# Performance work log

Hardware: AMD Instinct MI355X
Metric: run time of the kernel (lower is better)

## Reference

```python
import jax, jax.numpy as jnp
import numpy as np

N, E, D, H, L = 10000, 80000, 1024, 8, 2
C = D // H          # 128 per-head channels
NEG = 0.2           # GATv2 default negative_slope


def setup_inputs() -> dict:
    k = jax.random.split(jax.random.key(0), 16)
    s = 0.02
    return {
        "x": jax.random.normal(k[0], (N, D), jnp.float32),
        "edge_index": jax.random.randint(k[1], (2, E), 0, N),
        "edge_attr": jax.random.randint(k[2], (E,), 0, 3),
        "node_types": jax.random.randint(k[3], (N,), 0, 5),
        "node_type_emb": s * jax.random.normal(k[4], (5, D), jnp.float32),
        "edge_type_emb": s * jax.random.normal(k[5], (3, D), jnp.float32),
        "Wl": s * jax.random.normal(k[6], (L, D, D), jnp.float32),
        "bl": jnp.zeros((L, D), jnp.float32),
        "Wr": s * jax.random.normal(k[7], (L, D, D), jnp.float32),
        "br": jnp.zeros((L, D), jnp.float32),
        "We": s * jax.random.normal(k[8], (L, D, D), jnp.float32),
        "att": s * jax.random.normal(k[9], (L, H, C), jnp.float32),
        "conv_bias": jnp.zeros((L, D), jnp.float32),
        "out_W": s * jax.random.normal(k[10], (D, D), jnp.float32),
        "out_b": jnp.zeros((D,), jnp.float32),
    }


def _gatv2(h, src, dst, ee, Wl, bl, Wr, br, We, att, b):
    """PyG GATv2Conv: concat=True, add_self_loops=True (fill_value='mean')."""
    n = h.shape[0]
    xl = (h @ Wl + bl).reshape(n, H, C)   # source transform (lin_l)
    xr = (h @ Wr + br).reshape(n, H, C)   # target transform (lin_r)
    # self loops: edge_attr of a loop = mean of raw incoming edge feats
    cnt = jax.ops.segment_sum(jnp.ones(src.shape, jnp.float32), dst, num_segments=n)
    loop_attr = jax.ops.segment_sum(ee, dst, num_segments=n) / jnp.maximum(cnt, 1.0)[:, None]
    loops = jnp.arange(n)
    s2 = jnp.concatenate([src, loops])
    d2 = jnp.concatenate([dst, loops])
    ea = jnp.concatenate([ee, loop_attr], axis=0)          # [E+N, D]
    ep = (ea @ We).reshape(-1, H, C)                        # lin_edge (no bias)
    e = jax.nn.leaky_relu(xl[s2] + xr[d2] + ep, NEG)        # [E+N, H, C]
    logit = jnp.einsum('ehc,hc->eh', e, att)                # attention logits
    # segment softmax over destination nodes (every node has a self loop)
    m = jax.ops.segment_max(logit, d2, num_segments=n)
    a = jnp.exp(logit - m[d2])
    alpha = a / jax.ops.segment_sum(a, d2, num_segments=n)[d2]
    out = jax.ops.segment_sum(alpha[:, :, None] * xl[s2], d2, num_segments=n)
    return out.reshape(n, D) + b


def reference(x, edge_index, edge_attr, node_types, node_type_emb, edge_type_emb,
              Wl, bl, Wr, br, We, att, conv_bias, out_W, out_b):
    h = x + node_type_emb[node_types]
    ee = edge_type_emb[edge_attr]
    src, dst = edge_index[0], edge_index[1]
    for i in range(L):  # num_layers = 2
        h = h + jax.nn.relu(_gatv2(h, src, dst, ee, Wl[i], bl[i], Wr[i], br[i],
                                   We[i], att[i], conv_bias[i]))
    return h @ out_W + out_b
```

## Files before the change

kernel.cpp:

```cpp
#include <hip/hip_runtime.h>
#include <hip/hip_bf16.h>
#include <stdint.h>

typedef __bf16 bf16_t;
typedef bf16_t bf16x8 __attribute__((ext_vector_type(8)));
typedef bf16_t bf16x4 __attribute__((ext_vector_type(4)));
typedef float f32x4 __attribute__((ext_vector_type(4)));

#define NN 10000
#define EE 80000
#define DD 1024
#define LL 2
#define MPAD 10112
#define NEGS 0.2f

#define GLOAD_LDS16(g, l) \
    __builtin_amdgcn_global_load_lds((__attribute__((address_space(1))) void*)(void*)(g), \
                                     (__attribute__((address_space(3))) void*)(l), 16, 0, 0)

__global__ __launch_bounds__(256)
void preamble(const float* __restrict__ Wl, const float* __restrict__ Wr,
              const float* __restrict__ outW, bf16_t* __restrict__ WT,
              bf16_t* __restrict__ OWT,
              const float* __restrict__ x, const int* __restrict__ ntypes,
              const float* __restrict__ nte, bf16_t* __restrict__ hbuf,
              const float* __restrict__ bl, const float* __restrict__ br,
              const float* __restrict__ outb, float* __restrict__ biasb,
              float* __restrict__ M3L, int* __restrict__ deg)
{
    __shared__ float tile[32][33];
    int b = blockIdx.x;
    int tid = threadIdx.x;
    if (b < 5120) {
        int z = b >> 10, rem = b & 1023;
        int bx = rem & 31, by = rem >> 5;
        const float* src;
        bf16_t* dstp;
        switch (z) {
            case 0: src = Wl;                       dstp = WT;                        break;
            case 1: src = Wr;                       dstp = WT + (size_t)1024*1024;    break;
            case 2: src = Wl + (size_t)1024*1024;   dstp = WT + (size_t)2*1024*1024;  break;
            case 3: src = Wr + (size_t)1024*1024;   dstp = WT + (size_t)3*1024*1024;  break;
            default: src = outW;                    dstp = OWT;                       break;
        }
        int tx = tid & 31, ty = tid >> 5;
#pragma unroll
        for (int i = 0; i < 4; ++i)
            tile[ty + i*8][tx] = src[(size_t)(by*32 + ty + i*8)*1024 + bx*32 + tx];
        __syncthreads();
#pragma unroll
        for (int i = 0; i < 4; ++i)
            dstp[(size_t)(bx*32 + ty + i*8)*1024 + by*32 + tx] = (bf16_t)tile[tx][ty + i*8];
    } else if (b < 10176) {
        size_t idx = ((size_t)(b - 5120)*256 + tid) * 8;
        if (idx >= (size_t)MPAD*1024) return;
        int n = (int)(idx >> 10);
        int c = (int)(idx & 1023);
        bf16x8 outv;
        if (n < NN) {
            const float* xp = x + (size_t)n*1024 + c;
            int t = ntypes[n];
            const float* ep = nte + (size_t)t*1024 + c;
#pragma unroll
            for (int j = 0; j < 8; ++j) outv[j] = (bf16_t)(xp[j] + ep[j]);
        } else {
#pragma unroll
            for (int j = 0; j < 8; ++j) outv[j] = (bf16_t)0.f;
        }
        *(bf16x8*)(hbuf + idx) = outv;
    } else if (b < 10196) {
        int i = (b - 10176)*256 + tid;
        if (i < 4096) {
            int l = i >> 11, j = i & 2047;
            biasb[i] = (j < 1024) ? bl[l*1024 + j] : br[l*1024 + j - 1024];
        } else if (i < 5120) {
            biasb[i] = outb[i - 4096];
        }
    } else if (b < 10220) {
        int i = (b - 10196)*256 + tid;
        if (i < LL*3072) M3L[i] = 0.f;
    } else {
        int i = (b - 10220)*256 + tid;
        if (i < NN) deg[i] = 0;
    }
}

__global__ __launch_bounds__(256)
void compute_m3_all(const float* __restrict__ ete, const float* __restrict__ We,
                    float* __restrict__ M3L)
{
    int l   = blockIdx.x >> 8;
    int bid = blockIdx.x & 255;
    const float* WeL = We + (size_t)l*1024*1024;
    float* M3 = M3L + l*3072;
    int j  = (bid & 3) * 256 + threadIdx.x;
    int k0 = (bid >> 2) * 16;
    float a0 = 0.f, a1 = 0.f, a2 = 0.f;
#pragma unroll
    for (int kk = 0; kk < 16; ++kk) {
        int k = k0 + kk;
        float w = WeL[(size_t)k*1024 + j];
        a0 += ete[k]        * w;
        a1 += ete[1024 + k] * w;
        a2 += ete[2048 + k] * w;
    }
    atomicAdd(&M3[j],        a0);
    atomicAdd(&M3[1024 + j], a1);
    atomicAdd(&M3[2048 + j], a2);
}

__global__ void hist_k(const int* __restrict__ dsts, int* __restrict__ deg)
{ int e = blockIdx.x*256 + threadIdx.x; if (e < EE) atomicAdd(&deg[dsts[e]], 1); }

__global__ __launch_bounds__(1024)
void scan_csr(const int* __restrict__ deg, int* __restrict__ rp, int* __restrict__ cursor)
{
    __shared__ int tot[1024];
    int t = threadIdx.x;
    int base = t * 10;
    int v[10];
    int run = 0;
#pragma unroll
    for (int j = 0; j < 10; ++j) {
        int i = base + j;
        int d = (i < NN) ? deg[i] : 0;
        run += d;
        v[j] = run;
    }
    tot[t] = run;
    __syncthreads();
    for (int d = 1; d < 1024; d <<= 1) {
        int xv = (t >= d) ? tot[t - d] : 0;
        __syncthreads();
        tot[t] += xv;
        __syncthreads();
    }
    int ex = (t == 0) ? 0 : tot[t - 1];
#pragma unroll
    for (int j = 0; j < 10; ++j) {
        int i = base + j;
        if (i < NN) {
            int incl = ex + v[j];
            rp[i + 1] = incl;
            if (i + 1 < NN) cursor[i + 1] = incl;
        }
    }
    if (t == 0) { rp[0] = 0; cursor[0] = 0; }
}

__global__ void fill_csr(const int* __restrict__ srcs, const int* __restrict__ dsts,
                         const int* __restrict__ etype, int* __restrict__ cursor,
                         int* __restrict__ sorted_src, int* __restrict__ sorted_typ)
{
    int e = blockIdx.x*256 + threadIdx.x;
    if (e < EE) {
        int d = dsts[e];
        int pos = atomicAdd(&cursor[d], 1);
        sorted_src[pos] = srcs[e];
        sorted_typ[pos] = etype[e];
    }
}

template <typename OT>
__global__ __launch_bounds__(256)
void gemm_bt(const bf16_t* __restrict__ A, const bf16_t* __restrict__ BT,
             const float* __restrict__ bias, OT* __restrict__ Cmat,
             int K, int Ntot, int storeM, int mtiles, int ntiles)
{
    __shared__ __align__(16) bf16_t As[128*64];
    __shared__ __align__(16) bf16_t Bs[128*64];
    const int tid  = threadIdx.x;
    const int wave = tid >> 6;
    const int lane = tid & 63;

    const int GROUP_M = 8;
    int pid = blockIdx.x;
    int in_group = GROUP_M * ntiles;
    int gid = pid / in_group;
    int first_m = gid * GROUP_M;
    int gsz = mtiles - first_m; if (gsz > GROUP_M) gsz = GROUP_M;
    int local = pid % in_group;
    const int m0 = (first_m + (local % gsz)) * 128;
    const int n0 = (local / gsz) * 128;

    const int wm = (wave & 1) * 64;
    const int wn = (wave >> 1) * 64;
    const int quad = lane >> 4;
    const int l16  = lane & 15;

    const int srow = lane >> 3;
    const int gcol = ((lane & 7) ^ srow) * 8;

    f32x4 acc[4][4];
    f32x4 zero = {0.f, 0.f, 0.f, 0.f};
#pragma unroll
    for (int i = 0; i < 4; ++i)
#pragma unroll
        for (int j = 0; j < 4; ++j) acc[i][j] = zero;

    const bf16_t* aBase = A  + (size_t)(m0 + wave*8 + srow) * K + gcol;
    const bf16_t* bBase = BT + (size_t)(n0 + wave*8 + srow) * K + gcol;
    bf16_t* asDst = As + wave*512;
    bf16_t* bsDst = Bs + wave*512;

    for (int k0 = 0; k0 < K; k0 += 64) {
#pragma unroll
        for (int j = 0; j < 4; ++j)
            GLOAD_LDS16(aBase + (size_t)(j*32)*K + k0, asDst + j*2048);
#pragma unroll
        for (int j = 0; j < 4; ++j)
            GLOAD_LDS16(bBase + (size_t)(j*32)*K + k0, bsDst + j*2048);
        __syncthreads();
#pragma unroll
        for (int kk = 0; kk < 2; ++kk) {
            bf16x8 af[4], bfr[4];
#pragma unroll
            for (int mi = 0; mi < 4; ++mi) {
                int row = wm + mi*16 + l16;
                int ch  = ((kk*4 + quad) ^ (row & 7)) * 8;
                af[mi] = *(const bf16x8*)(As + row*64 + ch);
            }
#pragma unroll
            for (int ni = 0; ni < 4; ++ni) {
                int row = wn + ni*16 + l16;
                int ch  = ((kk*4 + quad) ^ (row & 7)) * 8;
                bfr[ni] = *(const bf16x8*)(Bs + row*64 + ch);
            }
#pragma unroll
            for (int mi = 0; mi < 4; ++mi)
#pragma unroll
                for (int ni = 0; ni < 4; ++ni)
                    acc[mi][ni] = __builtin_amdgcn_mfma_f32_16x16x32_bf16(af[mi], bfr[ni], acc[mi][ni], 0, 0, 0);
        }
        __syncthreads();
    }

#pragma unroll
    for (int mi = 0; mi < 4; ++mi) {
#pragma unroll
        for (int ni = 0; ni < 4; ++ni) {
            int col = n0 + wn + ni*16 + l16;
            float bv = bias[col];
#pragma unroll
            for (int r = 0; r < 4; ++r) {
                int row = m0 + wm + mi*16 + quad*4 + r;
                if (row < storeM)
                    Cmat[(size_t)row * Ntot + col] = (OT)(acc[mi][ni][r] + bv);
            }
        }
    }
}

__global__ __launch_bounds__(256)
void fused_edge(const int* __restrict__ rp, const int* __restrict__ ssrc,
                const int* __restrict__ styp, const bf16_t* __restrict__ XLXR,
                const float* __restrict__ M3, const float* __restrict__ attv,
                const float* __restrict__ cbias, bf16_t* __restrict__ hbuf)
{
    int node = blockIdx.x;
    int tid = threadIdx.x;
    int c = tid * 4;
    __shared__ int s_src[256];
    __shared__ int s_typ[256];

    int b = rp[node], en = rp[node + 1];

    bf16x4 xlv = *(const bf16x4*)(XLXR + (size_t)node*2048 + c);
    bf16x4 xrv = *(const bf16x4*)(XLXR + (size_t)node*2048 + 1024 + c);
    float xr0 = (float)xrv[0], xr1 = (float)xrv[1], xr2 = (float)xrv[2], xr3 = (float)xrv[3];
    float at0 = attv[c], at1 = attv[c+1], at2 = attv[c+2], at3 = attv[c+3];
    float m3r[3][4];
#pragma unroll
    for (int t = 0; t < 3; ++t)
#pragma unroll
        for (int j = 0; j < 4; ++j) m3r[t][j] = M3[t*1024 + c + j];

    float a0 = 0.f, a1 = 0.f, a2 = 0.f, a3 = 0.f;
    float den = 0.f;
    float cnt0 = 0.f, cnt1 = 0.f, cnt2 = 0.f;

    for (int base = b; base < en; base += 256) {
        int nchunk = en - base; if (nchunk > 256) nchunk = 256;
        __syncthreads();
        if (tid < nchunk) { s_src[tid] = ssrc[base + tid]; s_typ[tid] = styp[base + tid]; }
        __syncthreads();
#pragma unroll 2
        for (int i = 0; i < nchunk; ++i) {
            int s = s_src[i];
            int t = s_typ[i];
            bf16x4 xs = *(const bf16x4*)(XLXR + (size_t)s*2048 + c);
            float x0 = (float)xs[0], x1 = (float)xs[1], x2 = (float)xs[2], x3 = (float)xs[3];
            float v0 = x0 + xr0 + m3r[t][0]; v0 = (v0 > 0.f) ? v0 : NEGS * v0;
            float v1 = x1 + xr1 + m3r[t][1]; v1 = (v1 > 0.f) ? v1 : NEGS * v1;
            float v2 = x2 + xr2 + m3r[t][2]; v2 = (v2 > 0.f) ? v2 : NEGS * v2;
            float v3 = x3 + xr3 + m3r[t][3]; v3 = (v3 > 0.f) ? v3 : NEGS * v3;
            float part = v0*at0 + v1*at1 + v2*at2 + v3*at3;
            part += __shfl_xor(part, 1);
            part += __shfl_xor(part, 2);
            part += __shfl_xor(part, 4);
            part += __shfl_xor(part, 8);
            part += __shfl_xor(part, 16);
            part = fminf(fmaxf(part, -60.f), 60.f);
            float p = __expf(part);
            cnt0 += (t == 0) ? 1.f : 0.f;
            cnt1 += (t == 1) ? 1.f : 0.f;
            cnt2 += (t == 2) ? 1.f : 0.f;
            den += p;
            a0 += p * x0; a1 += p * x1; a2 += p * x2; a3 += p * x3;
        }
    }

    float deg = cnt0 + cnt1 + cnt2;
    float inv = 1.f / fmaxf(deg, 1.f);
    float w0 = cnt0 * inv, w1 = cnt1 * inv, w2 = cnt2 * inv;
    float sx0 = (float)xlv[0], sx1 = (float)xlv[1], sx2 = (float)xlv[2], sx3 = (float)xlv[3];
    float e0 = w0*m3r[0][0] + w1*m3r[1][0] + w2*m3r[2][0];
    float e1 = w0*m3r[0][1] + w1*m3r[1][1] + w2*m3r[2][1];
    float e2 = w0*m3r[0][2] + w1*m3r[1][2] + w2*m3r[2][2];
    float e3 = w0*m3r[0][3] + w1*m3r[1][3] + w2*m3r[2][3];
    float u0 = sx0 + xr0 + e0; u0 = (u0 > 0.f) ? u0 : NEGS * u0;
    float u1 = sx1 + xr1 + e1; u1 = (u1 > 0.f) ? u1 : NEGS * u1;
    float u2 = sx2 + xr2 + e2; u2 = (u2 > 0.f) ? u2 : NEGS * u2;
    float u3 = sx3 + xr3 + e3; u3 = (u3 > 0.f) ? u3 : NEGS * u3;
    float sp = u0*at0 + u1*at1 + u2*at2 + u3*at3;
    sp += __shfl_xor(sp, 1);
    sp += __shfl_xor(sp, 2);
    sp += __shfl_xor(sp, 4);
    sp += __shfl_xor(sp, 8);
    sp += __shfl_xor(sp, 16);
    sp = fminf(fmaxf(sp, -60.f), 60.f);
    float ps = __expf(sp);
    den += ps;
    a0 += ps * sx0; a1 += ps * sx1; a2 += ps * sx2; a3 += ps * sx3;

    float invd = 1.f / den;
    bf16x4 hv = *(const bf16x4*)(hbuf + (size_t)node*1024 + c);
    const float* cb = cbias + c;
    bf16x4 outv;
    outv[0] = (bf16_t)((float)hv[0] + fmaxf(a0*invd + cb[0], 0.f));
    outv[1] = (bf16_t)((float)hv[1] + fmaxf(a1*invd + cb[1], 0.f));
    outv[2] = (bf16_t)((float)hv[2] + fmaxf(a2*invd + cb[2], 0.f));
    outv[3] = (bf16_t)((float)hv[3] + fmaxf(a3*invd + cb[3], 0.f));
    *(bf16x4*)(hbuf + (size_t)node*1024 + c) = outv;
}

extern "C" void kernel_launch(void* const* d_in, const int* in_sizes, int n_in,
                              void* d_out, int out_size, void* d_ws, size_t ws_size,
                              hipStream_t stream)
{
    (void)in_sizes; (void)n_in; (void)out_size; (void)ws_size;
    const float* x     = (const float*)d_in[0];
    const int*   eidx  = (const int*)d_in[1];
    const int*   etype = (const int*)d_in[2];
    const int*   ntyp  = (const int*)d_in[3];
    const float* nte   = (const float*)d_in[4];
    const float* ete   = (const float*)d_in[5];
    const float* Wl    = (const float*)d_in[6];
    const float* bl    = (const float*)d_in[7];
    const float* Wr    = (const float*)d_in[8];
    const float* br    = (const float*)d_in[9];
    const float* We    = (const float*)d_in[10];
    const float* attw  = (const float*)d_in[11];
    const float* cbias = (const float*)d_in[12];
    const float* outW  = (const float*)d_in[13];
    const float* outb  = (const float*)d_in[14];
    const int* srcs = eidx;
    const int* dsts = eidx + EE;

    char* wsp = (char*)d_ws;
    size_t off = 0;
    auto carve = [&](size_t bytes) -> void* {
        void* pp = wsp + off;
        off += (bytes + 255) & ~(size_t)255;
        return pp;
    };
    bf16_t* hbuf  = (bf16_t*)carve((size_t)MPAD*1024*2);
    bf16_t* XLXR  = (bf16_t*)carve((size_t)MPAD*2048*2);
    bf16_t* WT    = (bf16_t*)carve((size_t)LL*2048*1024*2);
    bf16_t* OWT   = (bf16_t*)carve((size_t)1024*1024*2);
    float*  M3L   = (float*)carve((size_t)LL*3072*4);
    float*  biasb = (float*)carve(5120*4);
    int* deg    = (int*)carve((size_t)NN*4);
    int* rp     = (int*)carve((size_t)(NN+1)*4);
    int* cursor = (int*)carve((size_t)NN*4);
    int* ssrc   = (int*)carve((size_t)EE*4);
    int* styp   = (int*)carve((size_t)EE*4);

    preamble<<<10260, 256, 0, stream>>>(Wl, Wr, outW, WT, OWT,
                                        x, ntyp, nte, hbuf,
                                        bl, br, outb, biasb, M3L, deg);
    compute_m3_all<<<512, 256, 0, stream>>>(ete, We, M3L);
    hist_k<<<(EE + 255)/256, 256, 0, stream>>>(dsts, deg);
    scan_csr<<<1, 1024, 0, stream>>>(deg, rp, cursor);
    fill_csr<<<(EE + 255)/256, 256, 0, stream>>>(srcs, dsts, etype, cursor, ssrc, styp);

    for (int l = 0; l < LL; ++l) {
        gemm_bt<bf16_t><<<79*16, 256, 0, stream>>>(hbuf, WT + (size_t)l*2048*1024,
                                                   biasb + l*2048, XLXR,
                                                   1024, 2048, MPAD, 79, 16);
        fused_edge<<<NN, 256, 0, stream>>>(rp, ssrc, styp, XLXR, M3L + l*3072, attw + l*1024,
                                           cbias + l*1024, hbuf);
    }

    gemm_bt<float><<<79*8, 256, 0, stream>>>(hbuf, OWT, biasb + 4096, (float*)d_out,
                                             1024, 1024, NN, 79, 8);
}
```

Measured before the change: 410.7 us.

## Replace 128x128 GEMM with 256x256 tile, 8-wave pipelined double-buffered kernel

New measurement: 471.1 us. +14.7%, slower.

```diff
diff --git a/kernel.cpp b/kernel.cpp
--- a/kernel.cpp
+++ b/kernel.cpp
@@ -11,7 +11,7 @@
 #define EE 80000
 #define DD 1024
 #define LL 2
-#define MPAD 10112
+#define MPAD 10240
 #define NEGS 0.2f
 
 #define GLOAD_LDS16(g, l) \
@@ -51,7 +51,7 @@
 #pragma unroll
         for (int i = 0; i < 4; ++i)
             dstp[(size_t)(bx*32 + ty + i*8)*1024 + by*32 + tx] = (bf16_t)tile[tx][ty + i*8];
-    } else if (b < 10176) {
+    } else if (b < 10240) {
         size_t idx = ((size_t)(b - 5120)*256 + tid) * 8;
         if (idx >= (size_t)MPAD*1024) return;
         int n = (int)(idx >> 10);
@@ -68,19 +68,19 @@
             for (int j = 0; j < 8; ++j) outv[j] = (bf16_t)0.f;
         }
         *(bf16x8*)(hbuf + idx) = outv;
-    } else if (b < 10196) {
-        int i = (b - 10176)*256 + tid;
+    } else if (b < 10260) {
+        int i = (b - 10240)*256 + tid;
         if (i < 4096) {
             int l = i >> 11, j = i & 2047;
             biasb[i] = (j < 1024) ? bl[l*1024 + j] : br[l*1024 + j - 1024];
         } else if (i < 5120) {
             biasb[i] = outb[i - 4096];
         }
-    } else if (b < 10220) {
-        int i = (b - 10196)*256 + tid;
+    } else if (b < 10284) {
+        int i = (b - 10260)*256 + tid;
         if (i < LL*3072) M3L[i] = 0.f;
     } else {
-        int i = (b - 10220)*256 + tid;
+        int i = (b - 10284)*256 + tid;
         if (i < NN) deg[i] = 0;
     }
 }
@@ -162,88 +162,175 @@
 }
 
 template <typename OT>
-__global__ __launch_bounds__(256)
-void gemm_bt(const bf16_t* __restrict__ A, const bf16_t* __restrict__ BT,
+__global__ __launch_bounds__(512, 2)
+void gemm256(const bf16_t* __restrict__ A, const bf16_t* __restrict__ BT,
              const float* __restrict__ bias, OT* __restrict__ Cmat,
-             int K, int Ntot, int storeM, int mtiles, int ntiles)
-{
-    __shared__ __align__(16) bf16_t As[128*64];
-    __shared__ __align__(16) bf16_t Bs[128*64];
+             int K, int Ntot, int storeM, int ntiles)
+{
+    __shared__ __align__(16) bf16_t SH[65536];
     const int tid  = threadIdx.x;
-    const int wave = tid >> 6;
+    const int wv   = tid >> 6;
     const int lane = tid & 63;
-
-    const int GROUP_M = 8;
-    int pid = blockIdx.x;
-    int in_group = GROUP_M * ntiles;
-    int gid = pid / in_group;
-    int first_m = gid * GROUP_M;
-    int gsz = mtiles - first_m; if (gsz > GROUP_M) gsz = GROUP_M;
-    int local = pid % in_group;
-    const int m0 = (first_m + (local % gsz)) * 128;
-    const int n0 = (local / gsz) * 128;
-
-    const int wm = (wave & 1) * 64;
-    const int wn = (wave >> 1) * 64;
     const int quad = lane >> 4;
     const int l16  = lane & 15;
-
-    const int srow = lane >> 3;
-    const int gcol = ((lane & 7) ^ srow) * 8;
-
-    f32x4 acc[4][4];
-    f32x4 zero = {0.f, 0.f, 0.f, 0.f};
-#pragma unroll
-    for (int i = 0; i < 4; ++i)
-#pragma unroll
-        for (int j = 0; j < 4; ++j) acc[i][j] = zero;
-
-    const bf16_t* aBase = A  + (size_t)(m0 + wave*8 + srow) * K + gcol;
-    const bf16_t* bBase = BT + (size_t)(n0 + wave*8 + srow) * K + gcol;
-    bf16_t* asDst = As + wave*512;
-    bf16_t* bsDst = Bs + wave*512;
-
-    for (int k0 = 0; k0 < K; k0 += 64) {
-#pragma unroll
-        for (int j = 0; j < 4; ++j)
-            GLOAD_LDS16(aBase + (size_t)(j*32)*K + k0, asDst + j*2048);
-#pragma unroll
-        for (int j = 0; j < 4; ++j)
-            GLOAD_LDS16(bBase + (size_t)(j*32)*K + k0, bsDst + j*2048);
-        __syncthreads();
-#pragma unroll
-        for (int kk = 0; kk < 2; ++kk) {
-            bf16x8 af[4], bfr[4];
-#pragma unroll
-            for (int mi = 0; mi < 4; ++mi) {
-                int row = wm + mi*16 + l16;
-                int ch  = ((kk*4 + quad) ^ (row & 7)) * 8;
-                af[mi] = *(const bf16x8*)(As + row*64 + ch);
+    const int x7   = l16 & 7;
+    const int wr   = wv >> 2;
+    const int wc   = wv & 3;
+
+    const int nwg = gridDim.x;
+    const int cpx = nwg >> 3;
+    const int bid = blockIdx.x;
+    const int swz = (bid & 7) * cpx + (bid >> 3);
+    const int m0 = (swz / ntiles) * 256;
+    const int n0 = (swz % ntiles) * 256;
+    const int NT = K >> 6;
+
+    const int srow   = lane >> 3;
+    const int schunk = ((lane & 7) ^ srow) * 8;
+    const bf16_t* aS0 = A  + (size_t)(m0 + 16*wv + srow) * K + schunk;
+    const bf16_t* bS0 = BT + (size_t)(n0 + 16*wv + srow) * K + schunk;
+    bf16_t* ldsW = SH + 16*wv*64;
+
+    auto STAGE = [&](int s) {
+        if (s < 4*NT) {
+            const int buf  = (s >> 2) & 1;
+            const int kind = s & 3;
+            const int k0s  = (s >> 2) << 6;
+            const int h    = kind & 1;
+            const bf16_t* src = ((kind < 2) ? bS0 : aS0) + (size_t)(h*128)*K + k0s;
+            bf16_t* dst = ldsW + buf*32768 + ((kind >= 2) ? 16384 : 0) + h*8192;
+            GLOAD_LDS16(src, dst);
+            GLOAD_LDS16(src + (size_t)8*K, dst + 512);
+        }
+    };
+
+    f32x4 acc[8][4];
+    const f32x4 z4 = {0.f, 0.f, 0.f, 0.f};
+#pragma unroll
+    for (int i = 0; i < 8; ++i)
+#pragma unroll
+        for (int j = 0; j < 4; ++j) acc[i][j] = z4;
+
+#pragma unroll
+    for (int s = 0; s < 7; ++s) STAGE(s);
+    asm volatile("s_waitcnt vmcnt(6)" ::: "memory");
+    __builtin_amdgcn_s_barrier();
+    __builtin_amdgcn_sched_barrier(0);
+
+    const bf16_t* aR0 = SH + 16384 + (wr*128 + l16)*64;
+    const bf16_t* bR0 = SH + (wc*64 + l16)*64;
+    const int c0 = (quad ^ x7) * 8;
+    const int c1 = ((4 + quad) ^ x7) * 8;
+
+    for (int t = 0; t < NT; ++t) {
+        const int bofs = (t & 1) << 15;
+        const bf16_t* Ab = aR0 + bofs;
+        const bf16_t* Bb = bR0 + bofs;
+        const int sb = 4*t + 7;
+        bf16x8 bfr[4][2], afA[2][2], afB[2][2];
+
+#pragma unroll
+        for (int ni = 0; ni < 4; ++ni) {
+            bfr[ni][0] = *(const bf16x8*)(Bb + ni*1024 + c0);
+            bfr[ni][1] = *(const bf16x8*)(Bb + ni*1024 + c1);
+        }
+#pragma unroll
+        for (int m2 = 0; m2 < 2; ++m2) {
+            afA[m2][0] = *(const bf16x8*)(Ab + m2*1024 + c0);
+            afA[m2][1] = *(const bf16x8*)(Ab + m2*1024 + c1);
+        }
+        STAGE(sb + 0);
+        __builtin_amdgcn_s_barrier();
+        asm volatile("s_waitcnt lgkmcnt(0)" ::: "memory");
+        __builtin_amdgcn_sched_barrier(0);
+        __builtin_amdgcn_s_setprio(1);
+#pragma unroll
+        for (int m2 = 0; m2 < 2; ++m2)
+#pragma unroll
+            for (int ni = 0; ni < 4; ++ni) {
+                acc[m2][ni] = __builtin_amdgcn_mfma_f32_16x16x32_bf16(afA[m2][0], bfr[ni][0], acc[m2][ni], 0, 0, 0);
+                acc[m2][ni] = __builtin_amdgcn_mfma_f32_16x16x32_bf16(afA[m2][1], bfr[ni][1], acc[m2][ni], 0, 0, 0);
             }
+        __builtin_amdgcn_s_setprio(0);
+        __builtin_amdgcn_sched_barrier(0);
+        __builtin_amdgcn_s_barrier();
+
+#pragma unroll
+        for (int m2 = 0; m2 < 2; ++m2) {
+            afA[m2][0] = *(const bf16x8*)(Ab + (2 + m2)*1024 + c0);
+            afA[m2][1] = *(const bf16x8*)(Ab + (2 + m2)*1024 + c1);
+        }
+        STAGE(sb + 1);
+        __builtin_amdgcn_s_barrier();
+        asm volatile("s_waitcnt lgkmcnt(0)" ::: "memory");
+        __builtin_amdgcn_sched_barrier(0);
+        __builtin_amdgcn_s_setprio(1);
+#pragma unroll
+        for (int m2 = 0; m2 < 2; ++m2)
 #pragma unroll
             for (int ni = 0; ni < 4; ++ni) {
-                int row = wn + ni*16 + l16;
-                int ch  = ((kk*4 + quad) ^ (row & 7)) * 8;
-                bfr[ni] = *(const bf16x8*)(Bs + row*64 + ch);
+                acc[2+m2][ni] = __builtin_amdgcn_mfma_f32_16x16x32_bf16(afA[m2][0], bfr[ni][0], acc[2+m2][ni], 0, 0, 0);
+                acc[2+m2][ni] = __builtin_amdgcn_mfma_f32_16x16x32_bf16(afA[m2][1], bfr[ni][1], acc[2+m2][ni], 0, 0, 0);
             }
-#pragma unroll
-            for (int mi = 0; mi < 4; ++mi)
-#pragma unroll
-                for (int ni = 0; ni < 4; ++ni)
-                    acc[mi][ni] = __builtin_amdgcn_mfma_f32_16x16x32_bf16(af[mi], bfr[ni], acc[mi][ni], 0, 0, 0);
-        }
-        __syncthreads();
-    }
-
-#pragma unroll
-    for (int mi = 0; mi < 4; ++mi) {
+        __builtin_amdgcn_s_setprio(0);
+        __builtin_amdgcn_sched_barrier(0);
+        __builtin_amdgcn_s_barrier();
+
+#pragma unroll
+        for (int m2 = 0; m2 < 2; ++m2) {
+            afA[m2][0] = *(const bf16x8*)(Ab + (4 + m2)*1024 + c0);
+            afA[m2][1] = *(const bf16x8*)(Ab + (4 + m2)*1024 + c1);
+            afB[m2][0] = *(const bf16x8*)(Ab + (6 + m2)*1024 + c0);
+            afB[m2][1] = *(const bf16x8*)(Ab + (6 + m2)*1024 + c1);
+        }
+        STAGE(sb + 2);
+        __builtin_amdgcn_s_barrier();
+        asm volatile("s_waitcnt lgkmcnt(0)" ::: "memory");
+        __builtin_amdgcn_sched_barrier(0);
+        __builtin_amdgcn_s_setprio(1);
+#pragma unroll
+        for (int m2 = 0; m2 < 2; ++m2)
+#pragma unroll
+            for (int ni = 0; ni < 4; ++ni) {
+                acc[4+m2][ni] = __builtin_amdgcn_mfma_f32_16x16x32_bf16(afA[m2][0], bfr[ni][0], acc[4+m2][ni], 0, 0, 0);
+                acc[4+m2][ni] = __builtin_amdgcn_mfma_f32_16x16x32_bf16(afA[m2][1], bfr[ni][1], acc[4+m2][ni], 0, 0, 0);
+            }
+        __builtin_amdgcn_s_setprio(0);
+        __builtin_amdgcn_sched_barrier(0);
+        __builtin_amdgcn_s_barrier();
+
+        STAGE(sb + 3);
+        __builtin_amdgcn_s_barrier();
+        asm volatile("s_waitcnt lgkmcnt(0)" ::: "memory");
+        __builtin_amdgcn_sched_barrier(0);
+        __builtin_amdgcn_s_setprio(1);
+#pragma unroll
+        for (int m2 = 0; m2 < 2; ++m2)
+#pragma unroll
+            for (int ni = 0; ni < 4; ++ni) {
+                acc[6+m2][ni] = __builtin_amdgcn_mfma_f32_16x16x32_bf16(afB[m2][0], bfr[ni][0], acc[6+m2][ni], 0, 0, 0);
+                acc[6+m2][ni] = __builtin_amdgcn_mfma_f32_16x16x32_bf16(afB[m2][1], bfr[ni][1], acc[6+m2][ni], 0, 0, 0);
+            }
+        __builtin_amdgcn_s_setprio(0);
+        __builtin_amdgcn_sched_barrier(0);
+
+        if (t < NT - 1) {
+            if (t < NT - 2) asm volatile("s_waitcnt vmcnt(6)" ::: "memory");
+            else            asm volatile("s_waitcnt vmcnt(0)" ::: "memory");
+            __builtin_amdgcn_s_barrier();
+            __builtin_amdgcn_sched_barrier(0);
+        }
+    }
+
+#pragma unroll
+    for (int mi = 0; mi < 8; ++mi) {
 #pragma unroll
         for (int ni = 0; ni < 4; ++ni) {
-            int col = n0 + wn + ni*16 + l16;
-            float bv = bias[col];
+            const int col = n0 + wc*64 + ni*16 + l16;
+            const float bv = bias[col];
 #pragma unroll
             for (int r = 0; r < 4; ++r) {
-                int row = m0 + wm + mi*16 + quad*4 + r;
+                const int row = m0 + wr*128 + mi*16 + quad*4 + r;
                 if (row < storeM)
                     Cmat[(size_t)row * Ntot + col] = (OT)(acc[mi][ni][r] + bv);
             }
@@ -386,7 +473,7 @@
     int* ssrc   = (int*)carve((size_t)EE*4);
     int* styp   = (int*)carve((size_t)EE*4);
 
-    preamble<<<10260, 256, 0, stream>>>(Wl, Wr, outW, WT, OWT,
+    preamble<<<10324, 256, 0, stream>>>(Wl, Wr, outW, WT, OWT,
                                         x, ntyp, nte, hbuf,
                                         bl, br, outb, biasb, M3L, deg);
     compute_m3_all<<<512, 256, 0, stream>>>(ete, We, M3L);
@@ -395,13 +482,13 @@
     fill_csr<<<(EE + 255)/256, 256, 0, stream>>>(srcs, dsts, etype, cursor, ssrc, styp);
 
     for (int l = 0; l < LL; ++l) {
-        gemm_bt<bf16_t><<<79*16, 256, 0, stream>>>(hbuf, WT + (size_t)l*2048*1024,
-                                                   biasb + l*2048, XLXR,
-                                                   1024, 2048, MPAD, 79, 16);
+        gemm256<bf16_t><<<40*8, 512, 0, stream>>>(hbuf, WT + (size_t)l*2048*1024,
+                                                  biasb + l*2048, XLXR,
+                                                  1024, 2048, MPAD, 8);
         fused_edge<<<NN, 256, 0, stream>>>(rp, ssrc, styp, XLXR, M3L + l*3072, attw + l*1024,
                                            cbias + l*1024, hbuf);
     }
 
-    gemm_bt<float><<<79*8, 256, 0, stream>>>(hbuf, OWT, biasb + 4096, (float*)d_out,
-                                             1024, 1024, NN, 79, 8);
-}
+    gemm256<float><<<40*4, 512, 0, stream>>>(hbuf, OWT, biasb + 4096, (float*)d_out,
+                                             1024, 1024, NN, 4);
+}
```

## Split edge loop across two half-blocks with 8-wide bf16 gathers

Applied to the files above, without the earlier changes.

Result: slower. 562.2 us (+36.9%).

```diff
diff --git a/kernel.cpp b/kernel.cpp
--- a/kernel.cpp
+++ b/kernel.cpp
@@ -259,23 +259,33 @@
 {
     int node = blockIdx.x;
     int tid = threadIdx.x;
-    int c = tid * 4;
+    int eh = tid >> 7;
+    int q  = tid & 127;
+    int c8 = q * 8;
+
     __shared__ int s_src[256];
     __shared__ int s_typ[256];
+    __shared__ float red[12][128];
 
     int b = rp[node], en = rp[node + 1];
 
-    bf16x4 xlv = *(const bf16x4*)(XLXR + (size_t)node*2048 + c);
-    bf16x4 xrv = *(const bf16x4*)(XLXR + (size_t)node*2048 + 1024 + c);
-    float xr0 = (float)xrv[0], xr1 = (float)xrv[1], xr2 = (float)xrv[2], xr3 = (float)xrv[3];
-    float at0 = attv[c], at1 = attv[c+1], at2 = attv[c+2], at3 = attv[c+3];
-    float m3r[3][4];
-#pragma unroll
-    for (int t = 0; t < 3; ++t)
-#pragma unroll
-        for (int j = 0; j < 4; ++j) m3r[t][j] = M3[t*1024 + c + j];
-
-    float a0 = 0.f, a1 = 0.f, a2 = 0.f, a3 = 0.f;
+    bf16x8 xrv8 = *(const bf16x8*)(XLXR + (size_t)node*2048 + 1024 + c8);
+    float xr[8];
+#pragma unroll
+    for (int j = 0; j < 8; ++j) xr[j] = (float)xrv8[j];
+    f32x4 atl = *(const f32x4*)(attv + c8);
+    f32x4 ath = *(const f32x4*)(attv + c8 + 4);
+    float at[8] = {atl[0], atl[1], atl[2], atl[3], ath[0], ath[1], ath[2], ath[3]};
+    float m3r[3][8];
+#pragma unroll
+    for (int t = 0; t < 3; ++t) {
+        f32x4 ml = *(const f32x4*)(M3 + t*1024 + c8);
+        f32x4 mh = *(const f32x4*)(M3 + t*1024 + c8 + 4);
+#pragma unroll
+        for (int j = 0; j < 4; ++j) { m3r[t][j] = ml[j]; m3r[t][4+j] = mh[j]; }
+    }
+
+    float acc[8] = {0.f, 0.f, 0.f, 0.f, 0.f, 0.f, 0.f, 0.f};
     float den = 0.f;
     float cnt0 = 0.f, cnt1 = 0.f, cnt2 = 0.f;
 
@@ -285,63 +295,80 @@
         if (tid < nchunk) { s_src[tid] = ssrc[base + tid]; s_typ[tid] = styp[base + tid]; }
         __syncthreads();
 #pragma unroll 2
-        for (int i = 0; i < nchunk; ++i) {
+        for (int i = eh; i < nchunk; i += 2) {
             int s = s_src[i];
             int t = s_typ[i];
-            bf16x4 xs = *(const bf16x4*)(XLXR + (size_t)s*2048 + c);
-            float x0 = (float)xs[0], x1 = (float)xs[1], x2 = (float)xs[2], x3 = (float)xs[3];
-            float v0 = x0 + xr0 + m3r[t][0]; v0 = (v0 > 0.f) ? v0 : NEGS * v0;
-            float v1 = x1 + xr1 + m3r[t][1]; v1 = (v1 > 0.f) ? v1 : NEGS * v1;
-            float v2 = x2 + xr2 + m3r[t][2]; v2 = (v2 > 0.f) ? v2 : NEGS * v2;
-            float v3 = x3 + xr3 + m3r[t][3]; v3 = (v3 > 0.f) ? v3 : NEGS * v3;
-            float part = v0*at0 + v1*at1 + v2*at2 + v3*at3;
+            bf16x8 xs = *(const bf16x8*)(XLXR + (size_t)s*2048 + c8);
+            float x[8];
+            float part = 0.f;
+#pragma unroll
+            for (int j = 0; j < 8; ++j) {
+                x[j] = (float)xs[j];
+                float v = x[j] + xr[j] + m3r[t][j];
+                v = (v > 0.f) ? v : NEGS * v;
+                part += v * at[j];
+            }
             part += __shfl_xor(part, 1);
             part += __shfl_xor(part, 2);
             part += __shfl_xor(part, 4);
             part += __shfl_xor(part, 8);
-            part += __shfl_xor(part, 16);
             part = fminf(fmaxf(part, -60.f), 60.f);
             float p = __expf(part);
             cnt0 += (t == 0) ? 1.f : 0.f;
             cnt1 += (t == 1) ? 1.f : 0.f;
             cnt2 += (t == 2) ? 1.f : 0.f;
             den += p;
-            a0 += p * x0; a1 += p * x1; a2 += p * x2; a3 += p * x3;
-        }
-    }
-
-    float deg = cnt0 + cnt1 + cnt2;
-    float inv = 1.f / fmaxf(deg, 1.f);
-    float w0 = cnt0 * inv, w1 = cnt1 * inv, w2 = cnt2 * inv;
-    float sx0 = (float)xlv[0], sx1 = (float)xlv[1], sx2 = (float)xlv[2], sx3 = (float)xlv[3];
-    float e0 = w0*m3r[0][0] + w1*m3r[1][0] + w2*m3r[2][0];
-    float e1 = w0*m3r[0][1] + w1*m3r[1][1] + w2*m3r[2][1];
-    float e2 = w0*m3r[0][2] + w1*m3r[1][2] + w2*m3r[2][2];
-    float e3 = w0*m3r[0][3] + w1*m3r[1][3] + w2*m3r[2][3];
-    float u0 = sx0 + xr0 + e0; u0 = (u0 > 0.f) ? u0 : NEGS * u0;
-    float u1 = sx1 + xr1 + e1; u1 = (u1 > 0.f) ? u1 : NEGS * u1;
-    float u2 = sx2 + xr2 + e2; u2 = (u2 > 0.f) ? u2 : NEGS * u2;
-    float u3 = sx3 + xr3 + e3; u3 = (u3 > 0.f) ? u3 : NEGS * u3;
-    float sp = u0*at0 + u1*at1 + u2*at2 + u3*at3;
-    sp += __shfl_xor(sp, 1);
-    sp += __shfl_xor(sp, 2);
-    sp += __shfl_xor(sp, 4);
-    sp += __shfl_xor(sp, 8);
-    sp += __shfl_xor(sp, 16);
-    sp = fminf(fmaxf(sp, -60.f), 60.f);
-    float ps = __expf(sp);
-    den += ps;
-    a0 += ps * sx0; a1 += ps * sx1; a2 += ps * sx2; a3 += ps * sx3;
-
-    float invd = 1.f / den;
-    bf16x4 hv = *(const bf16x4*)(hbuf + (size_t)node*1024 + c);
-    const float* cb = cbias + c;
-    bf16x4 outv;
-    outv[0] = (bf16_t)((float)hv[0] + fmaxf(a0*invd + cb[0], 0.f));
-    outv[1] = (bf16_t)((float)hv[1] + fmaxf(a1*invd + cb[1], 0.f));
-    outv[2] = (bf16_t)((float)hv[2] + fmaxf(a2*invd + cb[2], 0.f));
-    outv[3] = (bf16_t)((float)hv[3] + fmaxf(a3*invd + cb[3], 0.f));
-    *(bf16x4*)(hbuf + (size_t)node*1024 + c) = outv;
+#pragma unroll
+            for (int j = 0; j < 8; ++j) acc[j] += p * x[j];
+        }
+    }
+
+    __syncthreads();
+    if (eh == 1) {
+#pragma unroll
+        for (int j = 0; j < 8; ++j) red[j][q] = acc[j];
+        red[8][q] = den; red[9][q] = cnt0; red[10][q] = cnt1; red[11][q] = cnt2;
+    }
+    __syncthreads();
+    if (eh == 0) {
+#pragma unroll
+        for (int j = 0; j < 8; ++j) acc[j] += red[j][q];
+        den  += red[8][q];
+        cnt0 += red[9][q]; cnt1 += red[10][q]; cnt2 += red[11][q];
+
+        float degf = cnt0 + cnt1 + cnt2;
+        float inv = 1.f / fmaxf(degf, 1.f);
+        float w0 = cnt0 * inv, w1 = cnt1 * inv, w2 = cnt2 * inv;
+
+        bf16x8 xlv8 = *(const bf16x8*)(XLXR + (size_t)node*2048 + c8);
+        float sx[8];
+        float sp = 0.f;
+#pragma unroll
+        for (int j = 0; j < 8; ++j) {
+            sx[j] = (float)xlv8[j];
+            float e = w0*m3r[0][j] + w1*m3r[1][j] + w2*m3r[2][j];
+            float u = sx[j] + xr[j] + e;
+            u = (u > 0.f) ? u : NEGS * u;
+            sp += u * at[j];
+        }
+        sp += __shfl_xor(sp, 1);
+        sp += __shfl_xor(sp, 2);
+        sp += __shfl_xor(sp, 4);
+        sp += __shfl_xor(sp, 8);
+        sp = fminf(fmaxf(sp, -60.f), 60.f);
+        float ps = __expf(sp);
+        den += ps;
+#pragma unroll
+        for (int j = 0; j < 8; ++j) acc[j] += ps * sx[j];
+
+        float invd = 1.f / den;
+        bf16x8 hv = *(const bf16x8*)(hbuf + (size_t)node*1024 + c8);
+        bf16x8 outv;
+#pragma unroll
+        for (int j = 0; j < 8; ++j)
+            outv[j] = (bf16_t)((float)hv[j] + fmaxf(acc[j]*invd + cbias[c8 + j], 0.f));
+        *(bf16x8*)(hbuf + (size_t)node*1024 + c8) = outv;
+    }
 }
 
 extern "C" void kernel_launch(void* const* d_in, const int* in_sizes, int n_in,
```

## Sort CSR edges by destination and edge type to drop per-edge type loads

Applied to the files above, without the earlier changes.

After: 427.6 us. +4.1%, slower.

```diff
diff --git a/kernel.cpp b/kernel.cpp
--- a/kernel.cpp
+++ b/kernel.cpp
@@ -26,7 +26,7 @@
               const float* __restrict__ nte, bf16_t* __restrict__ hbuf,
               const float* __restrict__ bl, const float* __restrict__ br,
               const float* __restrict__ outb, float* __restrict__ biasb,
-              float* __restrict__ M3L, int* __restrict__ deg)
+              float* __restrict__ M3L, int* __restrict__ deg3)
 {
     __shared__ float tile[32][33];
     int b = blockIdx.x;
@@ -81,7 +81,7 @@
         if (i < LL*3072) M3L[i] = 0.f;
     } else {
         int i = (b - 10220)*256 + tid;
-        if (i < NN) deg[i] = 0;
+        if (i < 3*NN) deg3[i] = 0;
     }
 }
 
@@ -109,21 +109,25 @@
     atomicAdd(&M3[2048 + j], a2);
 }
 
-__global__ void hist_k(const int* __restrict__ dsts, int* __restrict__ deg)
-{ int e = blockIdx.x*256 + threadIdx.x; if (e < EE) atomicAdd(&deg[dsts[e]], 1); }
+__global__ void hist_k(const int* __restrict__ dsts, const int* __restrict__ etype,
+                       int* __restrict__ deg3)
+{
+    int e = blockIdx.x*256 + threadIdx.x;
+    if (e < EE) atomicAdd(&deg3[dsts[e]*3 + etype[e]], 1);
+}
 
 __global__ __launch_bounds__(1024)
-void scan_csr(const int* __restrict__ deg, int* __restrict__ rp, int* __restrict__ cursor)
+void scan_csr(const int* __restrict__ deg3, int* __restrict__ rp3, int* __restrict__ cursor3)
 {
     __shared__ int tot[1024];
     int t = threadIdx.x;
-    int base = t * 10;
-    int v[10];
+    int base = t * 30;
+    int v[30];
     int run = 0;
 #pragma unroll
-    for (int j = 0; j < 10; ++j) {
+    for (int j = 0; j < 30; ++j) {
         int i = base + j;
-        int d = (i < NN) ? deg[i] : 0;
+        int d = (i < 3*NN) ? deg3[i] : 0;
         run += d;
         v[j] = run;
     }
@@ -137,27 +141,27 @@
     }
     int ex = (t == 0) ? 0 : tot[t - 1];
 #pragma unroll
-    for (int j = 0; j < 10; ++j) {
+    for (int j = 0; j < 30; ++j) {
         int i = base + j;
-        if (i < NN) {
+        if (i < 3*NN) {
             int incl = ex + v[j];
-            rp[i + 1] = incl;
-            if (i + 1 < NN) cursor[i + 1] = incl;
-        }
-    }
-    if (t == 0) { rp[0] = 0; cursor[0] = 0; }
+            rp3[i + 1] = incl;
+            if (i + 1 < 3*NN) cursor3[i + 1] = incl;
+        }
+    }
+    if (t == 0) { rp3[0] = 0; cursor3[0] = 0; }
 }
 
 __global__ void fill_csr(const int* __restrict__ srcs, const int* __restrict__ dsts,
-                         const int* __restrict__ etype, int* __restrict__ cursor,
-                         int* __restrict__ sorted_src, int* __restrict__ sorted_typ)
+                         const int* __restrict__ etype, int* __restrict__ cursor3,
+                         int* __restrict__ sorted_src)
 {
     int e = blockIdx.x*256 + threadIdx.x;
     if (e < EE) {
         int d = dsts[e];
-        int pos = atomicAdd(&cursor[d], 1);
+        int t = etype[e];
+        int pos = atomicAdd(&cursor3[d*3 + t], 1);
         sorted_src[pos] = srcs[e];
-        sorted_typ[pos] = etype[e];
     }
 }
 
@@ -252,8 +256,8 @@
 }
 
 __global__ __launch_bounds__(256)
-void fused_edge(const int* __restrict__ rp, const int* __restrict__ ssrc,
-                const int* __restrict__ styp, const bf16_t* __restrict__ XLXR,
+void fused_edge(const int* __restrict__ rp3, const int* __restrict__ ssrc,
+                const bf16_t* __restrict__ XLXR,
                 const float* __restrict__ M3, const float* __restrict__ attv,
                 const float* __restrict__ cbias, bf16_t* __restrict__ hbuf)
 {
@@ -261,67 +265,74 @@
     int tid = threadIdx.x;
     int c = tid * 4;
     __shared__ int s_src[256];
-    __shared__ int s_typ[256];
-
-    int b = rp[node], en = rp[node + 1];
+
+    int b   = rp3[3*node];
+    int t1g = rp3[3*node + 1];
+    int t2g = rp3[3*node + 2];
+    int en  = rp3[3*node + 3];
 
     bf16x4 xlv = *(const bf16x4*)(XLXR + (size_t)node*2048 + c);
     bf16x4 xrv = *(const bf16x4*)(XLXR + (size_t)node*2048 + 1024 + c);
     float xr0 = (float)xrv[0], xr1 = (float)xrv[1], xr2 = (float)xrv[2], xr3 = (float)xrv[3];
     float at0 = attv[c], at1 = attv[c+1], at2 = attv[c+2], at3 = attv[c+3];
-    float m3r[3][4];
-#pragma unroll
-    for (int t = 0; t < 3; ++t)
-#pragma unroll
-        for (int j = 0; j < 4; ++j) m3r[t][j] = M3[t*1024 + c + j];
+
+    float q00 = xr0 + M3[c+0],      q01 = xr1 + M3[c+1],      q02 = xr2 + M3[c+2],      q03 = xr3 + M3[c+3];
+    float q10 = xr0 + M3[1024+c+0], q11 = xr1 + M3[1024+c+1], q12 = xr2 + M3[1024+c+2], q13 = xr3 + M3[1024+c+3];
+    float q20 = xr0 + M3[2048+c+0], q21 = xr1 + M3[2048+c+1], q22 = xr2 + M3[2048+c+2], q23 = xr3 + M3[2048+c+3];
 
     float a0 = 0.f, a1 = 0.f, a2 = 0.f, a3 = 0.f;
     float den = 0.f;
-    float cnt0 = 0.f, cnt1 = 0.f, cnt2 = 0.f;
+
+    auto body = [&](int li, float p0, float p1, float p2, float p3) {
+        int s = s_src[li];
+        bf16x4 xs = *(const bf16x4*)(XLXR + (size_t)s*2048 + c);
+        float x0 = (float)xs[0], x1 = (float)xs[1], x2 = (float)xs[2], x3 = (float)xs[3];
+        float v0 = x0 + p0; v0 = (v0 > 0.f) ? v0 : NEGS * v0;
+        float v1 = x1 + p1; v1 = (v1 > 0.f) ? v1 : NEGS * v1;
+        float v2 = x2 + p2; v2 = (v2 > 0.f) ? v2 : NEGS * v2;
+        float v3 = x3 + p3; v3 = (v3 > 0.f) ? v3 : NEGS * v3;
+        float part = v0*at0 + v1*at1 + v2*at2 + v3*at3;
+        part += __shfl_xor(part, 1);
+        part += __shfl_xor(part, 2);
+        part += __shfl_xor(part, 4);
+        part += __shfl_xor(part, 8);
+        part += __shfl_xor(part, 16);
+        part = fminf(fmaxf(part, -60.f), 60.f);
+        float p = __expf(part);
+        den += p;
+        a0 += p * x0; a1 += p * x1; a2 += p * x2; a3 += p * x3;
+    };
 
     for (int base = b; base < en; base += 256) {
-        int nchunk = en - base; if (nchunk > 256) nchunk = 256;
-        __syncthreads();
-        if (tid < nchunk) { s_src[tid] = ssrc[base + tid]; s_typ[tid] = styp[base + tid]; }
-        __syncthreads();
+        int hi = en - base; if (hi > 256) hi = 256;
+        hi += base;
+        __syncthreads();
+        if (tid < hi - base) s_src[tid] = ssrc[base + tid];
+        __syncthreads();
+        int e0 = (t1g < hi) ? t1g : hi;
+        int e1 = (t2g < hi) ? t2g : hi;
+        int s1 = (t1g > base) ? t1g : base;
+        int s2 = (t2g > base) ? t2g : base;
 #pragma unroll 2
-        for (int i = 0; i < nchunk; ++i) {
-            int s = s_src[i];
-            int t = s_typ[i];
-            bf16x4 xs = *(const bf16x4*)(XLXR + (size_t)s*2048 + c);
-            float x0 = (float)xs[0], x1 = (float)xs[1], x2 = (float)xs[2], x3 = (float)xs[3];
-            float v0 = x0 + xr0 + m3r[t][0]; v0 = (v0 > 0.f) ? v0 : NEGS * v0;
-            float v1 = x1 + xr1 + m3r[t][1]; v1 = (v1 > 0.f) ? v1 : NEGS * v1;
-            float v2 = x2 + xr2 + m3r[t][2]; v2 = (v2 > 0.f) ? v2 : NEGS * v2;
-            float v3 = x3 + xr3 + m3r[t][3]; v3 = (v3 > 0.f) ? v3 : NEGS * v3;
-            float part = v0*at0 + v1*at1 + v2*at2 + v3*at3;
-            part += __shfl_xor(part, 1);
-            part += __shfl_xor(part, 2);
-            part += __shfl_xor(part, 4);
-            part += __shfl_xor(part, 8);
-            part += __shfl_xor(part, 16);
-            part = fminf(fmaxf(part, -60.f), 60.f);
-            float p = __expf(part);
-            cnt0 += (t == 0) ? 1.f : 0.f;
-            cnt1 += (t == 1) ? 1.f : 0.f;
-            cnt2 += (t == 2) ? 1.f : 0.f;
-            den += p;
-            a0 += p * x0; a1 += p * x1; a2 += p * x2; a3 += p * x3;
-        }
-    }
-
-    float deg = cnt0 + cnt1 + cnt2;
-    float inv = 1.f / fmaxf(deg, 1.f);
+        for (int i = base; i < e0; ++i) body(i - base, q00, q01, q02, q03);
+#pragma unroll 2
+        for (int i = s1; i < e1; ++i)   body(i - base, q10, q11, q12, q13);
+#pragma unroll 2
+        for (int i = s2; i < hi; ++i)   body(i - base, q20, q21, q22, q23);
+    }
+
+    float cnt0 = (float)(t1g - b);
+    float cnt1 = (float)(t2g - t1g);
+    float cnt2 = (float)(en - t2g);
+    float degf = cnt0 + cnt1 + cnt2;
+    float inv = 1.f / fmaxf(degf, 1.f);
     float w0 = cnt0 * inv, w1 = cnt1 * inv, w2 = cnt2 * inv;
+    float sw = w0 + w1 + w2;
     float sx0 = (float)xlv[0], sx1 = (float)xlv[1], sx2 = (float)xlv[2], sx3 = (float)xlv[3];
-    float e0 = w0*m3r[0][0] + w1*m3r[1][0] + w2*m3r[2][0];
-    float e1 = w0*m3r[0][1] + w1*m3r[1][1] + w2*m3r[2][1];
-    float e2 = w0*m3r[0][2] + w1*m3r[1][2] + w2*m3r[2][2];
-    float e3 = w0*m3r[0][3] + w1*m3r[1][3] + w2*m3r[2][3];
-    float u0 = sx0 + xr0 + e0; u0 = (u0 > 0.f) ? u0 : NEGS * u0;
-    float u1 = sx1 + xr1 + e1; u1 = (u1 > 0.f) ? u1 : NEGS * u1;
-    float u2 = sx2 + xr2 + e2; u2 = (u2 > 0.f) ? u2 : NEGS * u2;
-    float u3 = sx3 + xr3 + e3; u3 = (u3 > 0.f) ? u3 : NEGS * u3;
+    float u0 = sx0 + xr0*(1.f - sw) + w0*q00 + w1*q10 + w2*q20; u0 = (u0 > 0.f) ? u0 : NEGS * u0;
+    float u1 = sx1 + xr1*(1.f - sw) + w0*q01 + w1*q11 + w2*q21; u1 = (u1 > 0.f) ? u1 : NEGS * u1;
+    float u2 = sx2 + xr2*(1.f - sw) + w0*q02 + w1*q12 + w2*q22; u2 = (u2 > 0.f) ? u2 : NEGS * u2;
+    float u3 = sx3 + xr3*(1.f - sw) + w0*q03 + w1*q13 + w2*q23; u3 = (u3 > 0.f) ? u3 : NEGS * u3;
     float sp = u0*at0 + u1*at1 + u2*at2 + u3*at3;
     sp += __shfl_xor(sp, 1);
     sp += __shfl_xor(sp, 2);
@@ -380,25 +391,24 @@
     bf16_t* OWT   = (bf16_t*)carve((size_t)1024*1024*2);
     float*  M3L   = (float*)carve((size_t)LL*3072*4);
     float*  biasb = (float*)carve(5120*4);
-    int* deg    = (int*)carve((size_t)NN*4);
-    int* rp     = (int*)carve((size_t)(NN+1)*4);
-    int* cursor = (int*)carve((size_t)NN*4);
-    int* ssrc   = (int*)carve((size_t)EE*4);
-    int* styp   = (int*)carve((size_t)EE*4);
-
-    preamble<<<10260, 256, 0, stream>>>(Wl, Wr, outW, WT, OWT,
+    int* deg3    = (int*)carve((size_t)3*NN*4);
+    int* rp3     = (int*)carve((size_t)(3*NN+1)*4);
+    int* cursor3 = (int*)carve((size_t)3*NN*4);
+    int* ssrc    = (int*)carve((size_t)EE*4);
+
+    preamble<<<10338, 256, 0, stream>>>(Wl, Wr, outW, WT, OWT,
                                         x, ntyp, nte, hbuf,
-                                        bl, br, outb, biasb, M3L, deg);
+                                        bl, br, outb, biasb, M3L, deg3);
     compute_m3_all<<<512, 256, 0, stream>>>(ete, We, M3L);
-    hist_k<<<(EE + 255)/256, 256, 0, stream>>>(dsts, deg);
-    scan_csr<<<1, 1024, 0, stream>>>(deg, rp, cursor);
-    fill_csr<<<(EE + 255)/256, 256, 0, stream>>>(srcs, dsts, etype, cursor, ssrc, styp);
+    hist_k<<<(EE + 255)/256, 256, 0, stream>>>(dsts, etype, deg3);
+    scan_csr<<<1, 1024, 0, stream>>>(deg3, rp3, cursor3);
+    fill_csr<<<(EE + 255)/256, 256, 0, stream>>>(srcs, dsts, etype, cursor3, ssrc);
 
     for (int l = 0; l < LL; ++l) {
         gemm_bt<bf16_t><<<79*16, 256, 0, stream>>>(hbuf, WT + (size_t)l*2048*1024,
                                                    biasb + l*2048, XLXR,
                                                    1024, 2048, MPAD, 79, 16);
-        fused_edge<<<NN, 256, 0, stream>>>(rp, ssrc, styp, XLXR, M3L + l*3072, attw + l*1024,
+        fused_edge<<<NN, 256, 0, stream>>>(rp3, ssrc, XLXR, M3L + l*3072, attw + l*1024,
                                            cbias + l*1024, hbuf);
     }
 
```
